# Kernel optimization log

Hardware: AMD Instinct MI355X
Metric: run time of the kernel (lower is better)

Reference implementation:

```python
import jax, jax.numpy as jnp
import numpy as np

DEGREE = 8


def _askey_wilson_basis(x, a, b, c, d, q, degree):
    # Iterative 3-term recurrence (same math as the recursive torch version).
    # x: (batch, input_dim); a,b,c,d,q: scalars broadcast over x.
    basis = [jnp.ones_like(x)]
    if degree >= 1:
        p1 = (2 * (1 + a * b * q) * x - (a + b) * (1 + c * d * q)) / (1 + a * b * c * d * q ** 2)
        basis.append(p1)
    for n in range(2, degree + 1):
        An = (1 - a * b * q ** (n - 1)) * (1 - c * d * q ** (n - 1)) * (1 - a * b * c * d * q ** (2 * n - 2))
        An = An / ((1 - a * b * c * d * q ** (2 * n - 1)) * (1 - a * b * c * d * q ** (2 * n)))
        Cn = (1 - q ** n) * (1 - a * b * q ** (n - 1)) * (1 - c * d * q ** (n - 1)) * (1 - a * b * c * d * q ** (2 * n - 2))
        Cn = Cn / ((1 - a * b * c * d * q ** (2 * n - 2)) * (1 - a * b * c * d * q ** (2 * n - 1)))
        pn = ((2 * x - An) * basis[n - 1] - Cn * basis[n - 2]) / (1 - q ** n)
        basis.append(pn)
    return jnp.stack(basis, axis=-1)  # (batch, input_dim, degree+1)


def setup_inputs() -> dict:
    key = jax.random.key(0)
    k1, k2, k3, k4, k5, k6, k7 = jax.random.split(key, 7)
    input_dim, output_dim, degree = 1024, 1024, DEGREE
    batch = 8192
    x = jax.random.normal(k1, (batch, input_dim), dtype=jnp.float32)
    a = jax.random.normal(k2, (1,), dtype=jnp.float32)
    b = jax.random.normal(k3, (1,), dtype=jnp.float32)
    c = jax.random.normal(k4, (1,), dtype=jnp.float32)
    d = jax.random.normal(k5, (1,), dtype=jnp.float32)
    q = jax.random.normal(k6, (1,), dtype=jnp.float32)
    std = 1.0 / (input_dim * (degree + 1))
    coeffs = jax.random.normal(k7, (input_dim, output_dim, degree + 1), dtype=jnp.float32) * std
    return {"x": x, "a": a, "b": b, "c": c, "d": d, "q": q, "coeffs": coeffs}


def reference(x, a, b, c, d, q, coeffs) -> jnp.ndarray:
    a0, b0, c0, d0, q0 = a[0], b[0], c[0], d[0], q[0]
    basis = _askey_wilson_basis(x, a0, b0, c0, d0, q0, DEGREE)  # (b, i, d+1)
    y = jnp.einsum('bid,iod->bo', basis, coeffs)
    return y
```

## Files before the change

### kernel.cpp

```cpp
#include <hip/hip_runtime.h>
#include <cstdint>

typedef unsigned short u16;
typedef __bf16 bf16x8 __attribute__((ext_vector_type(8)));
typedef float f32x4 __attribute__((ext_vector_type(4)));

#define M_DIM 8192
#define N_DIM 1024
#define I_DIM 1024
#define NDEG 8
#define K_DIM (I_DIM * NDEG)
#define BM 256
#define BN 128
#define BK 64
#define NT (K_DIM / BK)
#define A_TILE (BM * BK)
#define B_TILE (BN * BK)

__device__ __forceinline__ u16 f2bf(float f) {
    union { float f; uint32_t u; } v; v.f = f;
    return (u16)((v.u + 0x7FFFu + ((v.u >> 16) & 1u)) >> 16);
}

__device__ __forceinline__ void gload_lds16(const u16* g, u16* l) {
    auto lp = reinterpret_cast<__attribute__((address_space(3))) uint32_t*>(
        reinterpret_cast<uintptr_t>(l));
    __builtin_amdgcn_global_load_lds(reinterpret_cast<const uint32_t*>(g), lp, 16, 0, 0);
}

__global__ __launch_bounds__(256) void aw_transform(
    const float* __restrict__ coeffs, u16* __restrict__ Bt, float* __restrict__ bias)
{
    __shared__ float lds[32][292];
    int bi = blockIdx.x >> 5, bo = blockIdx.x & 31;
    int i0 = bi * 32, o0 = bo * 32;
    int t = threadIdx.x;

    {
        int r = t >> 3, s = t & 7;
        const float4* src = (const float4*)(coeffs + ((size_t)(i0 + r) * N_DIM + o0) * 9);
#pragma unroll
        for (int j = 0; j < 9; ++j) {
            float4 v = src[s * 9 + j];
            *(float4*)&lds[r][(s * 9 + j) * 4] = v;
        }
    }
    __syncthreads();

    {
        int c = t >> 3, s2 = t & 7;
        u16 ob[32];
#pragma unroll
        for (int rr = 0; rr < 4; ++rr)
#pragma unroll
            for (int dd = 0; dd < 8; ++dd)
                ob[rr * 8 + dd] = f2bf(lds[s2 * 4 + rr][c * 9 + 1 + dd]);
        uint4* dst = (uint4*)(Bt + (size_t)(o0 + c) * K_DIM + (size_t)i0 * 8 + s2 * 32);
        const uint4* sp = (const uint4*)ob;
#pragma unroll
        for (int u = 0; u < 4; ++u) dst[u] = sp[u];
    }

    if (t < 32) {
        float sum = 0.f;
#pragma unroll
        for (int rr = 0; rr < 32; ++rr) sum += lds[rr][t * 9];
        atomicAdd(&bias[o0 + t], sum);
    }
}

__global__ void aw_basis(const float* __restrict__ x,
                         const float* __restrict__ pa, const float* __restrict__ pb,
                         const float* __restrict__ pc, const float* __restrict__ pd,
                         const float* __restrict__ pq,
                         u16* __restrict__ A, int row0)
{
    int t  = blockIdx.x * 256 + threadIdx.x;
    int rb = t >> 7;
    int g  = t & 127;
    int i0 = g << 3;
    int b  = row0 + rb;

    float a = *pa, bb = *pb, c = *pc, d = *pd, q = *pq;
    float ab = a * bb, cd = c * d, abcd = ab * cd;

    float qp[17];
    qp[0] = 1.f;
#pragma unroll
    for (int k = 1; k <= 16; ++k) qp[k] = qp[k - 1] * q;

    float den1 = 1.f + abcd * q * q;
    float c1x = 2.f * (1.f + ab * q) / den1;
    float c1c = -(a + bb) * (1.f + cd * q) / den1;

    float An[9], Cn[9], Sn[9];
#pragma unroll
    for (int n = 2; n <= 8; ++n) {
        float t1 = 1.f - ab * qp[n - 1];
        float t2 = 1.f - cd * qp[n - 1];
        float t3 = 1.f - abcd * qp[2 * n - 2];
        float t4 = 1.f - abcd * qp[2 * n - 1];
        float t5 = 1.f - abcd * qp[2 * n];
        An[n] = (t1 * t2 * t3) / (t4 * t5);
        Cn[n] = ((1.f - qp[n]) * t1 * t2 * t3) / (t3 * t4);
        Sn[n] = 1.f / (1.f - qp[n]);
    }

    const float4* x4 = (const float4*)(x + (size_t)b * I_DIM + i0);
    float4 v0 = x4[0], v1 = x4[1];
    float xv[8] = {v0.x, v0.y, v0.z, v0.w, v1.x, v1.y, v1.z, v1.w};

    u16 ob[64];
#pragma unroll
    for (int j = 0; j < 8; ++j) {
        float xj = xv[j];
        float p1 = c1x * xj + c1c;
        ob[j * 8 + 0] = f2bf(p1);
        float pm2 = 1.f, pm1 = p1;
#pragma unroll
        for (int n = 2; n <= 8; ++n) {
            float pn = ((2.f * xj - An[n]) * pm1 - Cn[n] * pm2) * Sn[n];
            ob[j * 8 + n - 1] = f2bf(pn);
            pm2 = pm1; pm1 = pn;
        }
    }

    uint4* dst = (uint4*)(A + (size_t)rb * K_DIM + (size_t)i0 * 8);
    const uint4* s = (const uint4*)ob;
#pragma unroll
    for (int u = 0; u < 8; ++u) dst[u] = s[u];
}

__global__ __launch_bounds__(512) void aw_gemm(
    const u16* __restrict__ A,
    const u16* __restrict__ B,
    const float* __restrict__ bias,
    float* __restrict__ C,
    int row0, int rowBlocks)
{
    __shared__ u16 As[3 * A_TILE];
    __shared__ u16 Bs[3 * B_TILE];

    int nwg = rowBlocks * 8;
    int bid = blockIdx.x;
    int per = nwg >> 3;
    int logical = (bid & 7) * per + (bid >> 3);
    int rowBlk = logical >> 3;
    int colBlk = logical & 7;

    const int tid  = threadIdx.x;
    const int lane = tid & 63;
    const int wid  = tid >> 6;
    const int wr = wid & 3;
    const int wc = wid >> 2;

    const u16* gA[4]; const u16* gB[2];
    int ldsA[4], ldsB[2];
#pragma unroll
    for (int j = 0; j < 4; ++j) {
        int idx = j * 512 + tid;
        int r = idx >> 3, sl = idx & 7;
        gA[j] = A + (size_t)rowBlk * BM * K_DIM + (size_t)r * K_DIM + ((sl ^ (r & 7)) << 3);
        ldsA[j] = idx << 3;
    }
#pragma unroll
    for (int j = 0; j < 2; ++j) {
        int idx = j * 512 + tid;
        int r = idx >> 3, sl = idx & 7;
        gB[j] = B + (size_t)colBlk * BN * K_DIM + (size_t)r * K_DIM + ((sl ^ (r & 7)) << 3);
        ldsB[j] = idx << 3;
    }

    int offA[2][4], offB[2][4];
#pragma unroll
    for (int ks = 0; ks < 2; ++ks) {
#pragma unroll
        for (int mi = 0; mi < 4; ++mi) {
            int r = wr * 64 + mi * 16 + (lane & 15);
            int s = ks * 4 + (lane >> 4);
            offA[ks][mi] = r * 128 + ((s ^ (r & 7)) << 4);
        }
#pragma unroll
        for (int ni = 0; ni < 4; ++ni) {
            int r = wc * 64 + ni * 16 + (lane & 15);
            int s = ks * 4 + (lane >> 4);
            offB[ks][ni] = r * 128 + ((s ^ (r & 7)) << 4);
        }
    }

    f32x4 acc[4][4];
#pragma unroll
    for (int mi = 0; mi < 4; ++mi)
#pragma unroll
        for (int ni = 0; ni < 4; ++ni)
            acc[mi][ni] = (f32x4){0.f, 0.f, 0.f, 0.f};

    auto stageHalf = [&](int kt, int buf, int half) {
        const int k0 = kt * BK;
        u16* dA = As + buf * A_TILE;
        u16* dB = Bs + buf * B_TILE;
        if (half == 0) {
            gload_lds16(gA[0] + k0, dA + ldsA[0]);
            gload_lds16(gA[1] + k0, dA + ldsA[1]);
            gload_lds16(gB[0] + k0, dB + ldsB[0]);
        } else {
            gload_lds16(gA[2] + k0, dA + ldsA[2]);
            gload_lds16(gA[3] + k0, dA + ldsA[3]);
            gload_lds16(gB[1] + k0, dB + ldsB[1]);
        }
    };

    stageHalf(0, 0, 0); stageHalf(0, 0, 1);
    stageHalf(1, 1, 0); stageHalf(1, 1, 1);
    asm volatile("s_waitcnt vmcnt(6)" ::: "memory");
    __builtin_amdgcn_s_barrier();

    int buf = 0;
    for (int t = 0; t < NT; ++t) {
        const char* aB = (const char*)(As + buf * A_TILE);
        const char* bB = (const char*)(Bs + buf * B_TILE);
        int nb = buf + 2; if (nb >= 3) nb -= 3;
        const bool pf = (t + 2 < NT);

        bf16x8 a0[4], b0[4];
#pragma unroll
        for (int mi = 0; mi < 4; ++mi) a0[mi] = *(const bf16x8*)(aB + offA[0][mi]);
#pragma unroll
        for (int ni = 0; ni < 4; ++ni) b0[ni] = *(const bf16x8*)(bB + offB[0][ni]);
        if (pf) stageHalf(t + 2, nb, 0);
        __builtin_amdgcn_s_barrier();
        __builtin_amdgcn_s_setprio(1);
#pragma unroll
        for (int mi = 0; mi < 4; ++mi)
#pragma unroll
            for (int ni = 0; ni < 4; ++ni)
                acc[mi][ni] = __builtin_amdgcn_mfma_f32_16x16x32_bf16(
                    a0[mi], b0[ni], acc[mi][ni], 0, 0, 0);
        __builtin_amdgcn_s_setprio(0);
        __builtin_amdgcn_s_barrier();

        bf16x8 a1[4], b1[4];
#pragma unroll
        for (int mi = 0; mi < 4; ++mi) a1[mi] = *(const bf16x8*)(aB + offA[1][mi]);
#pragma unroll
        for (int ni = 0; ni < 4; ++ni) b1[ni] = *(const bf16x8*)(bB + offB[1][ni]);
        if (pf) stageHalf(t + 2, nb, 1);
        __builtin_amdgcn_s_barrier();
        __builtin_amdgcn_s_setprio(1);
#pragma unroll
        for (int mi = 0; mi < 4; ++mi)
#pragma unroll
            for (int ni = 0; ni < 4; ++ni)
                acc[mi][ni] = __builtin_amdgcn_mfma_f32_16x16x32_bf16(
                    a1[mi], b1[ni], acc[mi][ni], 0, 0, 0);
        __builtin_amdgcn_s_setprio(0);
        if (pf) { asm volatile("s_waitcnt vmcnt(6)" ::: "memory"); }
        else if (t + 1 < NT) { asm volatile("s_waitcnt vmcnt(0)" ::: "memory"); }
        __builtin_amdgcn_s_barrier();

        buf += 1; if (buf >= 3) buf -= 3;
    }

    int gRow = row0 + rowBlk * BM + wr * 64;
    int gCol = colBlk * BN + wc * 64;
#pragma unroll
    for (int mi = 0; mi < 4; ++mi) {
#pragma unroll
        for (int ni = 0; ni < 4; ++ni) {
            int rr = gRow + mi * 16 + ((lane >> 4) << 2);
            int cc = gCol + ni * 16 + (lane & 15);
            float bv = bias[cc];
            float* dst = C + (size_t)rr * N_DIM + cc;
#pragma unroll
            for (int j = 0; j < 4; ++j) dst[(size_t)j * N_DIM] = acc[mi][ni][j] + bv;
        }
    }
}

extern "C" void kernel_launch(void* const* d_in, const int* in_sizes, int n_in,
                              void* d_out, int out_size, void* d_ws, size_t ws_size,
                              hipStream_t stream)
{
    const float* x      = (const float*)d_in[0];
    const float* pa     = (const float*)d_in[1];
    const float* pb     = (const float*)d_in[2];
    const float* pc     = (const float*)d_in[3];
    const float* pd     = (const float*)d_in[4];
    const float* pq     = (const float*)d_in[5];
    const float* coeffs = (const float*)d_in[6];
    float* out = (float*)d_out;

    float* bias = (float*)d_ws;
    const size_t biasBytes = 4096;
    u16* Bt = (u16*)((char*)d_ws + biasBytes);
    const size_t btBytes = (size_t)N_DIM * K_DIM * sizeof(u16);
    u16* Abuf = (u16*)((char*)d_ws + biasBytes + btBytes);
    size_t used = biasBytes + btBytes;
    size_t avail = ws_size > used ? ws_size - used : 0;

    int chunk = M_DIM;
    while (chunk > 256 && (size_t)chunk * K_DIM * sizeof(u16) > avail) chunk >>= 1;

    hipMemsetAsync(bias, 0, N_DIM * sizeof(float), stream);
    aw_transform<<<1024, 256, 0, stream>>>(coeffs, Bt, bias);

    for (int row0 = 0; row0 < M_DIM; row0 += chunk) {
        aw_basis<<<(chunk * 128) / 256, 256, 0, stream>>>(x, pa, pb, pc, pd, pq, Abuf, row0);
        int rowBlocks = chunk / BM;
        aw_gemm<<<rowBlocks * 8, 512, 0, stream>>>(Abuf, Bt, bias, out, row0, rowBlocks);
    }
}
```

Before: 190.3 us.

## Split K across wave groups with larger per-wave tiles and LDS reduction

Each wave now computes a 128x64 output sub-tile over half of each BK=64 slice. Two wave groups split the K dimension and their partial accumulators are reduced through LDS at the end. This halves the LDS fragment reads per MFMA, cuts the barriers per K-tile from three to two, and issues all prefetch loads at once. In exchange each wave holds 128 accumulator registers, which adds register pressure and may limit occupancy, and the epilogue gains a shared-memory reduction and a full block sync.

```diff
diff --git a/kernel.cpp b/kernel.cpp
--- a/kernel.cpp
+++ b/kernel.cpp
@@ -138,8 +138,9 @@
     float* __restrict__ C,
     int row0, int rowBlocks)
 {
-    __shared__ u16 As[3 * A_TILE];
-    __shared__ u16 Bs[3 * B_TILE];
+    __shared__ alignas(16) u16 smem[3 * A_TILE + 3 * B_TILE];
+    u16* As = smem;
+    u16* Bs = smem + 3 * A_TILE;
 
     int nwg = rowBlocks * 8;
     int bid = blockIdx.x;
@@ -151,8 +152,10 @@
     const int tid  = threadIdx.x;
     const int lane = tid & 63;
     const int wid  = tid >> 6;
-    const int wr = wid & 3;
-    const int wc = wid >> 2;
+    const int quad = wid & 3;
+    const int wr   = quad >> 1;
+    const int wc   = quad & 1;
+    const int myKs = wid >> 2;
 
     const u16* gA[4]; const u16* gB[2];
     int ldsA[4], ldsB[2];
@@ -171,47 +174,41 @@
         ldsB[j] = idx << 3;
     }
 
-    int offA[2][4], offB[2][4];
-#pragma unroll
-    for (int ks = 0; ks < 2; ++ks) {
-#pragma unroll
-        for (int mi = 0; mi < 4; ++mi) {
-            int r = wr * 64 + mi * 16 + (lane & 15);
-            int s = ks * 4 + (lane >> 4);
-            offA[ks][mi] = r * 128 + ((s ^ (r & 7)) << 4);
-        }
-#pragma unroll
-        for (int ni = 0; ni < 4; ++ni) {
-            int r = wc * 64 + ni * 16 + (lane & 15);
-            int s = ks * 4 + (lane >> 4);
-            offB[ks][ni] = r * 128 + ((s ^ (r & 7)) << 4);
-        }
-    }
-
-    f32x4 acc[4][4];
-#pragma unroll
-    for (int mi = 0; mi < 4; ++mi)
+    int offA[8], offB[4];
+#pragma unroll
+    for (int mi = 0; mi < 8; ++mi) {
+        int r = wr * 128 + mi * 16 + (lane & 15);
+        int s = myKs * 4 + (lane >> 4);
+        offA[mi] = r * 128 + ((s ^ (r & 7)) << 4);
+    }
+#pragma unroll
+    for (int ni = 0; ni < 4; ++ni) {
+        int r = wc * 64 + ni * 16 + (lane & 15);
+        int s = myKs * 4 + (lane >> 4);
+        offB[ni] = r * 128 + ((s ^ (r & 7)) << 4);
+    }
+
+    f32x4 acc[8][4];
+#pragma unroll
+    for (int mi = 0; mi < 8; ++mi)
 #pragma unroll
         for (int ni = 0; ni < 4; ++ni)
             acc[mi][ni] = (f32x4){0.f, 0.f, 0.f, 0.f};
 
-    auto stageHalf = [&](int kt, int buf, int half) {
+    auto stage = [&](int kt, int buf) {
         const int k0 = kt * BK;
         u16* dA = As + buf * A_TILE;
         u16* dB = Bs + buf * B_TILE;
-        if (half == 0) {
-            gload_lds16(gA[0] + k0, dA + ldsA[0]);
-            gload_lds16(gA[1] + k0, dA + ldsA[1]);
-            gload_lds16(gB[0] + k0, dB + ldsB[0]);
-        } else {
-            gload_lds16(gA[2] + k0, dA + ldsA[2]);
-            gload_lds16(gA[3] + k0, dA + ldsA[3]);
-            gload_lds16(gB[1] + k0, dB + ldsB[1]);
-        }
+        gload_lds16(gA[0] + k0, dA + ldsA[0]);
+        gload_lds16(gA[1] + k0, dA + ldsA[1]);
+        gload_lds16(gA[2] + k0, dA + ldsA[2]);
+        gload_lds16(gA[3] + k0, dA + ldsA[3]);
+        gload_lds16(gB[0] + k0, dB + ldsB[0]);
+        gload_lds16(gB[1] + k0, dB + ldsB[1]);
     };
 
-    stageHalf(0, 0, 0); stageHalf(0, 0, 1);
-    stageHalf(1, 1, 0); stageHalf(1, 1, 1);
+    stage(0, 0);
+    stage(1, 1);
     asm volatile("s_waitcnt vmcnt(6)" ::: "memory");
     __builtin_amdgcn_s_barrier();
 
@@ -222,57 +219,64 @@
         int nb = buf + 2; if (nb >= 3) nb -= 3;
         const bool pf = (t + 2 < NT);
 
-        bf16x8 a0[4], b0[4];
-#pragma unroll
-        for (int mi = 0; mi < 4; ++mi) a0[mi] = *(const bf16x8*)(aB + offA[0][mi]);
-#pragma unroll
-        for (int ni = 0; ni < 4; ++ni) b0[ni] = *(const bf16x8*)(bB + offB[0][ni]);
-        if (pf) stageHalf(t + 2, nb, 0);
+        bf16x8 fa[8], fb[4];
+#pragma unroll
+        for (int mi = 0; mi < 8; ++mi) fa[mi] = *(const bf16x8*)(aB + offA[mi]);
+#pragma unroll
+        for (int ni = 0; ni < 4; ++ni) fb[ni] = *(const bf16x8*)(bB + offB[ni]);
+
+        if (pf) stage(t + 2, nb);
         __builtin_amdgcn_s_barrier();
+
         __builtin_amdgcn_s_setprio(1);
 #pragma unroll
-        for (int mi = 0; mi < 4; ++mi)
+        for (int mi = 0; mi < 8; ++mi)
 #pragma unroll
             for (int ni = 0; ni < 4; ++ni)
                 acc[mi][ni] = __builtin_amdgcn_mfma_f32_16x16x32_bf16(
-                    a0[mi], b0[ni], acc[mi][ni], 0, 0, 0);
+                    fa[mi], fb[ni], acc[mi][ni], 0, 0, 0);
         __builtin_amdgcn_s_setprio(0);
+
+        if (pf)               { asm volatile("s_waitcnt vmcnt(6)" ::: "memory"); }
+        else if (t + 1 < NT)  { asm volatile("s_waitcnt vmcnt(0)" ::: "memory"); }
         __builtin_amdgcn_s_barrier();
 
-        bf16x8 a1[4], b1[4];
-#pragma unroll
-        for (int mi = 0; mi < 4; ++mi) a1[mi] = *(const bf16x8*)(aB + offA[1][mi]);
-#pragma unroll
-        for (int ni = 0; ni < 4; ++ni) b1[ni] = *(const bf16x8*)(bB + offB[1][ni]);
-        if (pf) stageHalf(t + 2, nb, 1);
-        __builtin_amdgcn_s_barrier();
-        __builtin_amdgcn_s_setprio(1);
-#pragma unroll
-        for (int mi = 0; mi < 4; ++mi)
+        buf += 1; if (buf >= 3) buf -= 3;
+    }
+
+    float* red = (float*)smem;
+    if (myKs == 1) {
+        f32x4* dst = (f32x4*)red + quad * 2048;
+#pragma unroll
+        for (int mi = 0; mi < 8; ++mi)
 #pragma unroll
             for (int ni = 0; ni < 4; ++ni)
-                acc[mi][ni] = __builtin_amdgcn_mfma_f32_16x16x32_bf16(
-                    a1[mi], b1[ni], acc[mi][ni], 0, 0, 0);
-        __builtin_amdgcn_s_setprio(0);
-        if (pf) { asm volatile("s_waitcnt vmcnt(6)" ::: "memory"); }
-        else if (t + 1 < NT) { asm volatile("s_waitcnt vmcnt(0)" ::: "memory"); }
-        __builtin_amdgcn_s_barrier();
-
-        buf += 1; if (buf >= 3) buf -= 3;
-    }
-
-    int gRow = row0 + rowBlk * BM + wr * 64;
-    int gCol = colBlk * BN + wc * 64;
-#pragma unroll
-    for (int mi = 0; mi < 4; ++mi) {
-#pragma unroll
-        for (int ni = 0; ni < 4; ++ni) {
-            int rr = gRow + mi * 16 + ((lane >> 4) << 2);
-            int cc = gCol + ni * 16 + (lane & 15);
-            float bv = bias[cc];
-            float* dst = C + (size_t)rr * N_DIM + cc;
-#pragma unroll
-            for (int j = 0; j < 4; ++j) dst[(size_t)j * N_DIM] = acc[mi][ni][j] + bv;
+                dst[(mi * 4 + ni) * 64 + lane] = acc[mi][ni];
+    }
+    __syncthreads();
+    if (myKs == 0) {
+        const f32x4* src = (const f32x4*)red + quad * 2048;
+#pragma unroll
+        for (int mi = 0; mi < 8; ++mi)
+#pragma unroll
+            for (int ni = 0; ni < 4; ++ni) {
+                f32x4 p = src[(mi * 4 + ni) * 64 + lane];
+                acc[mi][ni] += p;
+            }
+
+        int gRow = row0 + rowBlk * BM + wr * 128;
+        int gCol = colBlk * BN + wc * 64;
+#pragma unroll
+        for (int mi = 0; mi < 8; ++mi) {
+#pragma unroll
+            for (int ni = 0; ni < 4; ++ni) {
+                int rr = gRow + mi * 16 + ((lane >> 4) << 2);
+                int cc = gCol + ni * 16 + (lane & 15);
+                float bv = bias[cc];
+                float* dst = C + (size_t)rr * N_DIM + cc;
+#pragma unroll
+                for (int j = 0; j < 4; ++j) dst[(size_t)j * N_DIM] = acc[mi][ni][j] + bv;
+            }
         }
     }
 }
```

New measurement: 192.3 us. Within noise of the previous version (+1.1%).
